# Kernel tuning notes

Measured on AMD Instinct MI355X. Metric: run time of the kernel, lower is better.

The kernel has to match this reference:

```python
import jax, jax.numpy as jnp
import numpy as np

D = 512       # d_model
L = 4         # num_layers
NH = 4        # nhead (fixed in __init__)
HD = D // NH
FF = 2 * D    # dim_feedforward = d_model*2
A = 32        # action_dim
B = 1024
STEPS = 64
SF_TH = 2.0   # sf_threshold
ALPHA = 2.0   # ATan surrogate width


@jax.custom_vjp
def spike(v):
    # Heaviside spike; surrogate gradient defined below (standard SNN practice)
    return (v > 0.0).astype(v.dtype)

def _spike_fwd(v):
    return spike(v), v

def _spike_bwd(v, g):
    sg = ALPHA / (2.0 * (1.0 + (jnp.pi / 2.0 * ALPHA * v) ** 2))
    return (g * sg,)

spike.defvjp(_spike_fwd, _spike_bwd)


def layer_norm(x, g, b):
    m = jnp.mean(x, axis=-1, keepdims=True)
    v = jnp.var(x, axis=-1, keepdims=True)
    return (x - m) / jnp.sqrt(v + 1e-5) * g + b


def setup_inputs() -> dict:
    key = jax.random.key(0)
    ks = jax.random.split(key, 24)
    w = lambda k, shape: jax.random.normal(k, shape, jnp.float32) * 0.02
    return {
        'initial_state': jax.random.normal(ks[0], (B, D), jnp.float32),
        'action_sequence': jax.random.normal(ks[1], (B, STEPS, A), jnp.float32),
        # action encoder
        'Wa': w(ks[2], (A, D)), 'ba': jnp.zeros((D,), jnp.float32),
        # per-layer SFormerBlock params, stacked on leading L dim
        'ln1_g': jnp.ones((L, D), jnp.float32), 'ln1_b': jnp.zeros((L, D), jnp.float32),
        'Wq': w(ks[3], (L, D, D)), 'bq': jnp.zeros((L, D), jnp.float32),
        'Wk': w(ks[4], (L, D, D)), 'bk': jnp.zeros((L, D), jnp.float32),
        'Wv': w(ks[5], (L, D, D)), 'bv': jnp.zeros((L, D), jnp.float32),
        'Wo': w(ks[6], (L, D, D)), 'bo': jnp.zeros((L, D), jnp.float32),
        'ln2_g': jnp.ones((L, D), jnp.float32), 'ln2_b': jnp.zeros((L, D), jnp.float32),
        'Wf1': w(ks[7], (L, D, FF)), 'bf1': jnp.zeros((L, FF), jnp.float32),
        'Wf2': w(ks[8], (L, FF, D)), 'bf2': jnp.zeros((L, D), jnp.float32),
        # transition AdaptiveLIFNeuron per-feature threshold
        'lif_th': jnp.ones((D,), jnp.float32),
        # reward head
        'Wr': w(ks[9], (D, 1)), 'br': jnp.zeros((1,), jnp.float32),
    }


def reference(initial_state, action_sequence, Wa, ba, ln1_g, ln1_b, Wq, bq, Wk, bk, Wv, bv, Wo, bo, ln2_g, ln2_b, Wf1, bf1, Wf2, bf2, lif_th, Wr, br):
    scale = 1.0 / jnp.sqrt(jnp.asarray(HD, jnp.float32))

    def block(x, l):
        # x: [B, 1, D]
        h = layer_norm(x, ln1_g[l], ln1_b[l])
        b_ = x.shape[0]
        q = (h @ Wq[l] + bq[l]).reshape(b_, 1, NH, HD)
        k = (h @ Wk[l] + bk[l]).reshape(b_, 1, NH, HD)
        v = (h @ Wv[l] + bv[l]).reshape(b_, 1, NH, HD)
        scores = jnp.einsum('bqhd,bkhd->bhqk', q, k) * scale
        attn = jax.nn.softmax(scores, axis=-1)
        o = jnp.einsum('bhqk,bkhd->bqhd', attn, v).reshape(b_, 1, D)
        x = x + o @ Wo[l] + bo[l]
        h2 = layer_norm(x, ln2_g[l], ln2_b[l])
        # spiking FFN: heaviside at sf_threshold with surrogate grad
        x = x + spike(h2 @ Wf1[l] + bf1[l] - SF_TH) @ Wf2[l] + bf2[l]
        return x

    def step(state, a):
        # predict_next_step
        x = state + a @ Wa + ba            # [B, D]
        x = x[:, None, :]                  # [B, 1, D]
        for l in range(L):
            x = block(x, l)
        x = x[:, 0, :]
        next_state = spike(x - lif_th)     # transition_lif (single-step LIF: v = input)
        reward = next_state @ Wr + br      # [B, 1]
        return next_state, (next_state, reward)

    acts = jnp.swapaxes(action_sequence, 0, 1)  # [Steps, B, A]
    final_state, (S, R) = jax.lax.scan(step, initial_state, acts)
    states = jnp.swapaxes(S, 0, 1)    # [B, Steps, D]
    rewards = jnp.swapaxes(R, 0, 1)   # [B, Steps, 1]
    return states, rewards, final_state
```

## Files before the change

### kernel.cpp

```cpp
#include <hip/hip_runtime.h>

#define D_ 512
#define FF_ 1024
#define L_ 4
#define A_ 32
#define B_ 1024
#define STEPS_ 64
#define RB_ 0.0625f
#define RB8_ 0.15f

typedef __attribute__((ext_vector_type(8))) short bf16x8;
typedef __attribute__((ext_vector_type(4))) float f32x4;
typedef __attribute__((ext_vector_type(2))) unsigned long u64x2;
#define MFMA16(a,b,c) __builtin_amdgcn_mfma_f32_16x16x32_bf16(a,b,c,0,0,0)
#define MFMA8(a,b,c)  __builtin_amdgcn_mfma_f32_16x16x32_fp8_fp8((long)(a),(long)(b),(c),0,0,0)

__device__ __forceinline__ unsigned rne16(float f) {
    unsigned u = __float_as_uint(f);
    return (u + 0x7fffu + ((u >> 16) & 1u)) >> 16;
}
__device__ __forceinline__ float fb(unsigned hu) { return __uint_as_float(hu << 16); }

#define LD4(R0, R1, R2, R3, P0_, P1_, P2_, P3_)                                \
    asm volatile("global_load_dwordx4 %0, %4, off\n\t"                         \
                 "global_load_dwordx4 %1, %5, off\n\t"                         \
                 "global_load_dwordx4 %2, %6, off\n\t"                         \
                 "global_load_dwordx4 %3, %7, off"                             \
                 : "=&v"(R0), "=&v"(R1), "=&v"(R2), "=&v"(R3)                  \
                 : "v"(P0_), "v"(P1_), "v"(P2_), "v"(P3_))

#define WAIT4(N, R0, R1, R2, R3)                                               \
    asm volatile("s_waitcnt vmcnt(" #N ")"                                     \
                 : "+v"(R0), "+v"(R1), "+v"(R2), "+v"(R3) :: "memory")

__global__ __launch_bounds__(256) void wvo_kernel(
    const float* __restrict__ Wv, const float* __restrict__ Wo,
    unsigned* __restrict__ Whi, unsigned* __restrict__ Wlo)
{
    __shared__ float wvt[16][D_];
    int bx  = blockIdx.x;
    int l   = bx >> 6;
    int rem = bx & 63;
    int k0  = (rem >> 1) * 16;
    int n   = (rem & 1) * 256 + threadIdx.x;

    const float* wvbase = Wv + (size_t)l * D_ * D_ + (size_t)k0 * D_;
    for (int idx = threadIdx.x; idx < 16 * D_; idx += 256)
        wvt[idx >> 9][idx & (D_ - 1)] = wvbase[idx];
    __syncthreads();

    float acc[16];
#pragma unroll
    for (int kk = 0; kk < 16; ++kk) acc[kk] = 0.f;

    const float* wop = Wo + (size_t)l * D_ * D_ + n;
    for (int m = 0; m < D_; m += 4) {
        float w0 = wop[(m + 0) * D_];
        float w1 = wop[(m + 1) * D_];
        float w2 = wop[(m + 2) * D_];
        float w3 = wop[(m + 3) * D_];
#pragma unroll
        for (int kk = 0; kk < 16; ++kk) {
            float4 wv4 = *(const float4*)&wvt[kk][m];
            acc[kk] += wv4.x * w0 + wv4.y * w1 + wv4.z * w2 + wv4.w * w3;
        }
    }
    int nt = n >> 4, ln15 = n & 15;
    int kkblk = k0 >> 5;
    int gbase = (k0 & 31) >> 3;
#pragma unroll
    for (int gi = 0; gi < 2; ++gi) {
        int lane_s = ((gbase + gi) << 4) | ln15;
        size_t fbase = ((((size_t)l * 32 + nt) * 16 + kkblk) * 64 + lane_s) * 4;
#pragma unroll
        for (int jp = 0; jp < 4; ++jp) {
            float v0 = acc[gi * 8 + jp * 2], v1 = acc[gi * 8 + jp * 2 + 1];
            unsigned h0 = rne16(v0), h1 = rne16(v1);
            Whi[fbase + jp] = h0 | (h1 << 16);
            float r0 = v0 - fb(h0), r1 = v1 - fb(h1);
            Wlo[fbase + jp] = rne16(r0) | (rne16(r1) << 16);
        }
    }
}

__global__ __launch_bounds__(256) void bvo_kernel(
    const float* __restrict__ bv, const float* __restrict__ bo,
    const float* __restrict__ Wo, float* __restrict__ bvo)
{
    int l = blockIdx.x >> 1;
    int n = (blockIdx.x & 1) * 256 + threadIdx.x;
    float acc = bo[l * D_ + n];
    const float* wop = Wo + (size_t)l * D_ * D_ + n;
    const float* bvp = bv + l * D_;
    for (int m = 0; m < D_; ++m) acc += bvp[m] * wop[m * D_];
    bvo[l * D_ + n] = acc;
}

__global__ __launch_bounds__(64) void packwf1_fp8(
    const float* __restrict__ Wf1, unsigned char* __restrict__ Pf8)
{
    int bid = blockIdx.x;
    int lane = threadIdx.x;
    int l  = bid >> 9;
    int nt = (bid >> 3) & 63;
    int p  = bid & 7;
    int n  = nt * 16 + (lane & 15);
    unsigned w[4];
#pragma unroll
    for (int half = 0; half < 2; ++half) {
        int kk = 2 * p + half;
        int krow = kk * 32 + (lane >> 4) * 8;
        const float* src = Wf1 + ((size_t)l * D_ + krow) * FF_ + n;
        float f0 = src[0 * FF_] * 16.f, f1 = src[1 * FF_] * 16.f;
        float f2 = src[2 * FF_] * 16.f, f3 = src[3 * FF_] * 16.f;
        float f4 = src[4 * FF_] * 16.f, f5 = src[5 * FF_] * 16.f;
        float f6 = src[6 * FF_] * 16.f, f7 = src[7 * FF_] * 16.f;
        unsigned lo = 0, hi = 0;
        lo = __builtin_amdgcn_cvt_pk_fp8_f32(f0, f1, lo, false);
        lo = __builtin_amdgcn_cvt_pk_fp8_f32(f2, f3, lo, true);
        hi = __builtin_amdgcn_cvt_pk_fp8_f32(f4, f5, hi, false);
        hi = __builtin_amdgcn_cvt_pk_fp8_f32(f6, f7, hi, true);
        w[half * 2] = lo; w[half * 2 + 1] = hi;
    }
    uint4 o; o.x = w[0]; o.y = w[1]; o.z = w[2]; o.w = w[3];
    ((uint4*)Pf8)[((size_t)(l * 64 + nt) * 8 + p) * 64 + lane] = o;
}

__device__ __forceinline__ void layer_norm_frag(
    float (*xb)[D_], unsigned* __restrict__ afrag,
    const float* __restrict__ g, const float* __restrict__ bt,
    float (*red)[4][2], int sg, int r)
{
    int c = 2 * r;
    float v0 = xb[sg][c], v1 = xb[sg][c + 1];
    float s  = v0 + v1;
    float ss = v0 * v0 + v1 * v1;
#pragma unroll
    for (int m = 1; m < 64; m <<= 1) {
        s  += __shfl_xor(s, m);
        ss += __shfl_xor(ss, m);
    }
    if ((r & 63) == 0) { red[sg][r >> 6][0] = s; red[sg][r >> 6][1] = ss; }
    __syncthreads();
    float S  = red[sg][0][0] + red[sg][1][0] + red[sg][2][0] + red[sg][3][0];
    float SS = red[sg][0][1] + red[sg][1][1] + red[sg][2][1] + red[sg][3][1];
    float mean = S * (1.f / 512.f);
    float var  = SS * (1.f / 512.f) - mean * mean;
    float rstd = 1.0f / sqrtf(var + 1e-5f);
    float h0 = (v0 - mean) * rstd * g[c]     + bt[c];
    float h1 = (v1 - mean) * rstd * g[c + 1] + bt[c + 1];
    unsigned u0 = rne16(h0), u1 = rne16(h1);
    float l0 = h0 - fb(u0), l1 = h1 - fb(u1);
    int kk = c >> 5, grp = (c & 31) >> 3, jp = (c & 7) >> 1;
    afrag[(kk * 64 + ((grp << 4) | sg))       * 4 + jp] = u0 | (u1 << 16);
    afrag[(kk * 64 + ((grp << 4) | (sg + 4))) * 4 + jp] = rne16(l0) | (rne16(l1) << 16);
    __syncthreads();
}

__device__ __forceinline__ void ln2_pack8(
    float (*xb)[D_], unsigned short* __restrict__ afrag8,
    const float* __restrict__ g, const float* __restrict__ bt,
    float (*red)[4][2], float* __restrict__ ln2m, float* __restrict__ ln2r,
    int sg, int r)
{
    int c = 2 * r;
    float v0 = xb[sg][c], v1 = xb[sg][c + 1];
    float s  = v0 + v1;
    float ss = v0 * v0 + v1 * v1;
#pragma unroll
    for (int m = 1; m < 64; m <<= 1) {
        s  += __shfl_xor(s, m);
        ss += __shfl_xor(ss, m);
    }
    if ((r & 63) == 0) { red[sg][r >> 6][0] = s; red[sg][r >> 6][1] = ss; }
    __syncthreads();
    float S  = red[sg][0][0] + red[sg][1][0] + red[sg][2][0] + red[sg][3][0];
    float SS = red[sg][0][1] + red[sg][1][1] + red[sg][2][1] + red[sg][3][1];
    float mean = S * (1.f / 512.f);
    float var  = SS * (1.f / 512.f) - mean * mean;
    float rstd = 1.0f / sqrtf(var + 1e-5f);
    if (r == 0) { ln2m[sg] = mean; ln2r[sg] = rstd; }
    float h0 = (v0 - mean) * rstd * g[c]     + bt[c];
    float h1 = (v1 - mean) * rstd * g[c + 1] + bt[c + 1];
    unsigned u = __builtin_amdgcn_cvt_pk_fp8_f32(h0, h1, 0, false);
    int kk = c >> 5, grp = (c & 31) >> 3, j = c & 7;
    afrag8[(kk * 64 + ((grp << 4) | sg)) * 4 + (j >> 1)] = (unsigned short)u;
    __syncthreads();
}

__global__ __launch_bounds__(1024)
__attribute__((amdgpu_waves_per_eu(4, 4)))
void smain(
    const float* __restrict__ init_state,
    const float* __restrict__ acts,
    const float* __restrict__ Wa,  const float* __restrict__ ba,
    const float* __restrict__ ln1g, const float* __restrict__ ln1b,
    const float* __restrict__ ln2g, const float* __restrict__ ln2b,
    const float* __restrict__ Wf1, const float* __restrict__ bf1,
    const float* __restrict__ Wf2, const float* __restrict__ bf2,
    const float* __restrict__ lifth,
    const float* __restrict__ Wr,  const float* __restrict__ br,
    const unsigned* __restrict__ Whi, const unsigned* __restrict__ Wlo,
    const unsigned char* __restrict__ Pf8, const float* __restrict__ bvo,
    float* __restrict__ out_states, float* __restrict__ out_rewards,
    float* __restrict__ out_final)
{
    __shared__ __align__(16) unsigned afrag[16 * 64 * 4];
    __shared__ __align__(16) unsigned short afrag8[16 * 64 * 4];
    __shared__ __align__(16) float xb[4][D_];
    __shared__ float areg[4][A_];
    __shared__ float red[4][4][2];
    __shared__ float rr[16];
    __shared__ float ln2m[4], ln2r[4];
    __shared__ int   fire_cnt, resc_cnt;
    __shared__ int   fire_list[256];
    __shared__ int   rescue_list[64];

    const int tid  = threadIdx.x;
    const int sg   = tid >> 8;
    const int r    = tid & 255;
    const int wv   = tid >> 6;
    const int lane = tid & 63;
    const int b    = blockIdx.x * 4 + sg;

    float st0 = init_state[(size_t)b * D_ + r];
    float st1 = init_state[(size_t)b * D_ + r + 256];
#pragma unroll
    for (int z = 0; z < 4; ++z) afrag[tid + z * 1024] = 0;
    ((unsigned*)afrag8)[tid] = 0;
    ((unsigned*)afrag8)[tid + 1024] = 0;
    __syncthreads();

    for (int t = 0; t < STEPS_; ++t) {
        if (tid < 128) {
            int sg2 = tid >> 5, j = tid & 31;
            areg[sg2][j] = acts[((size_t)(blockIdx.x * 4 + sg2)) * (STEPS_ * A_) + t * A_ + j];
        }
        __syncthreads();

        {
            float x0 = st0 + ba[r];
            float x1 = st1 + ba[r + 256];
#pragma unroll
            for (int j = 0; j < A_; ++j) {
                float av = areg[sg][j];
                x0 += av * Wa[j * D_ + r];
                x1 += av * Wa[j * D_ + r + 256];
            }
            xb[sg][r] = x0; xb[sg][r + 256] = x1;
        }
        __syncthreads();

        for (int l = 0; l < L_; ++l) {
            layer_norm_frag(xb, afrag, ln1g + l * D_, ln1b + l * D_, red, sg, r);

            {
                const bf16x8* Ah = (const bf16x8*)afrag;
                const size_t lb = (size_t)l * (32 * 16 * 64);
                const bf16x8* BH0 = (const bf16x8*)Whi + lb + (size_t)(2 * wv) * (16 * 64) + lane;
                const bf16x8* BL0 = (const bf16x8*)Wlo + lb + (size_t)(2 * wv) * (16 * 64) + lane;
                const bf16x8* BH1 = BH0 + 16 * 64;
                const bf16x8* BL1 = BL0 + 16 * 64;
                f32x4 c1a = {0.f,0.f,0.f,0.f}, c2a = c1a, c1b = c1a, c2b = c1a;
                bf16x8 aH0, aG0, aH1, aG1;
                bf16x8 bH0, bG0, bH1, bG1;
                bf16x8 cH0, cG0, cH1, cG1;
#define G1LD(S, KK) LD4(S##H0, S##G0, S##H1, S##G1, \
                        BH0 + (KK) * 64, BL0 + (KK) * 64, BH1 + (KK) * 64, BL1 + (KK) * 64)
#define G1MM(S, KK) do { bf16x8 a_ = Ah[(KK) * 64 + lane]; \
    c1a = MFMA16(a_, S##H0, c1a); c2a = MFMA16(a_, S##G0, c2a); \
    c1b = MFMA16(a_, S##H1, c1b); c2b = MFMA16(a_, S##G1, c2b); } while (0)
#define G1W(N, S) WAIT4(N, S##H0, S##G0, S##H1, S##G1)
                G1LD(a, 0); G1LD(b, 1); G1LD(c, 2);
                G1W(8, a); G1MM(a, 0);  G1LD(a, 3);
                G1W(8, b); G1MM(b, 1);  G1LD(b, 4);
                G1W(8, c); G1MM(c, 2);  G1LD(c, 5);
                G1W(8, a); G1MM(a, 3);  G1LD(a, 6);
                G1W(8, b); G1MM(b, 4);  G1LD(b, 7);
                G1W(8, c); G1MM(c, 5);  G1LD(c, 8);
                G1W(8, a); G1MM(a, 6);  G1LD(a, 9);
                G1W(8, b); G1MM(b, 7);  G1LD(b, 10);
                G1W(8, c); G1MM(c, 8);  G1LD(c, 11);
                G1W(8, a); G1MM(a, 9);  G1LD(a, 12);
                G1W(8, b); G1MM(b, 10); G1LD(b, 13);
                G1W(8, c); G1MM(c, 11); G1LD(c, 14);
                G1W(8, a); G1MM(a, 12); G1LD(a, 15);
                G1W(8, b); G1MM(b, 13);
                G1W(4, c); G1MM(c, 14);
                G1W(0, a); G1MM(a, 15);
#undef G1LD
#undef G1MM
#undef G1W
                const int nt0 = 2 * wv, nt1 = nt0 + 1;
#pragma unroll
                for (int s = 0; s < 4; ++s) {
                    float pa = c1a[s] + c2a[s]; float qa = __shfl(pa, (lane & 15) + 16);
                    float pb = c1b[s] + c2b[s]; float qb = __shfl(pb, (lane & 15) + 16);
                    if (lane < 16) {
                        int ca = nt0 * 16 + lane, cb = nt1 * 16 + lane;
                        xb[s][ca] += pa + qa + bvo[l * D_ + ca];
                        xb[s][cb] += pb + qb + bvo[l * D_ + cb];
                    }
                }
            }
            __syncthreads();

            if (tid == 0) { fire_cnt = 0; resc_cnt = 0; }

            ln2_pack8(xb, afrag8, ln2g + l * D_, ln2b + l * D_, red, ln2m, ln2r, sg, r);

            {
                const unsigned long* Ah8 = (const unsigned long*)afrag8;
                const int m0 = 4 * wv;
                const u64x2* Q0 = (const u64x2*)Pf8 + ((size_t)(l * 64 + m0 + 0) * 8) * 64 + lane;
                const u64x2* Q1 = (const u64x2*)Pf8 + ((size_t)(l * 64 + m0 + 1) * 8) * 64 + lane;
                const u64x2* Q2 = (const u64x2*)Pf8 + ((size_t)(l * 64 + m0 + 2) * 8) * 64 + lane;
                const u64x2* Q3 = (const u64x2*)Pf8 + ((size_t)(l * 64 + m0 + 3) * 8) * 64 + lane;
                f32x4 p0 = {0.f,0.f,0.f,0.f}, p1 = p0, p2 = p0, p3 = p0;
                u64x2 aB0, aB1, aB2, aB3;
                u64x2 bB0, bB1, bB2, bB3;
                u64x2 cB0, cB1, cB2, cB3;
#define G2LD(S, P) LD4(S##B0, S##B1, S##B2, S##B3, \
                       Q0 + (P) * 64, Q1 + (P) * 64, Q2 + (P) * 64, Q3 + (P) * 64)
#define G2MM(S, P) do { \
    unsigned long a0_ = Ah8[(2 * (P))     * 64 + lane]; \
    unsigned long a1_ = Ah8[(2 * (P) + 1) * 64 + lane]; \
    p0 = MFMA8(a0_, S##B0.x, p0); p1 = MFMA8(a0_, S##B1.x, p1); \
    p2 = MFMA8(a0_, S##B2.x, p2); p3 = MFMA8(a0_, S##B3.x, p3); \
    p0 = MFMA8(a1_, S##B0.y, p0); p1 = MFMA8(a1_, S##B1.y, p1); \
    p2 = MFMA8(a1_, S##B2.y, p2); p3 = MFMA8(a1_, S##B3.y, p3); } while (0)
#define G2W(N, S) WAIT4(N, S##B0, S##B1, S##B2, S##B3)
                G2LD(a, 0); G2LD(b, 1); G2LD(c, 2);
                G2W(8, a); G2MM(a, 0); G2LD(a, 3);
                G2W(8, b); G2MM(b, 1); G2LD(b, 4);
                G2W(8, c); G2MM(c, 2); G2LD(c, 5);
                G2W(8, a); G2MM(a, 3); G2LD(a, 6);
                G2W(8, b); G2MM(b, 4); G2LD(b, 7);
                G2W(8, c); G2MM(c, 5);
                G2W(4, a); G2MM(a, 6);
                G2W(0, b); G2MM(b, 7);
#undef G2LD
#undef G2MM
#undef G2W
                const float* bf1g = bf1 + l * FF_;
#pragma unroll
                for (int s = 0; s < 4; ++s) {
                    float v0 = p0[s]; float w0 = __shfl(v0, (lane & 15) + 16);
                    float v1 = p1[s]; float w1 = __shfl(v1, (lane & 15) + 16);
                    float v2 = p2[s]; float w2 = __shfl(v2, (lane & 15) + 16);
                    float v3 = p3[s]; float w3 = __shfl(v3, (lane & 15) + 16);
                    if (lane < 16) {
#pragma unroll
                        for (int q = 0; q < 4; ++q) {
                            float sum = (q == 0) ? v0 + w0 : (q == 1) ? v1 + w1
                                       : (q == 2) ? v2 + w2 : v3 + w3;
                            int n = (m0 + q) * 16 + lane;
                            float pr = sum * 0.0625f + bf1g[n] - 2.0f;
                            if (pr > RB8_) {
                                int idx = atomicAdd(&fire_cnt, 1);
                                if (idx < 256) fire_list[idx] = (s << 12) | n;
                            } else if (pr > -RB8_) {
                                int idx = atomicAdd(&resc_cnt, 1);
                                if (idx < 64) rescue_list[idx] = (s << 12) | n;
                            }
                        }
                    }
                }
            }
            __syncthreads();

            {
                int rc = resc_cnt; if (rc > 64) rc = 64;
                const float* g2 = ln2g + l * D_;
                const float* b2 = ln2b + l * D_;
                for (int e = 0; e < rc; ++e) {
                    int ent = rescue_list[e];
                    int i = ent >> 12, n = ent & 4095;
                    float p = 0.f;
                    if (tid < D_) {
                        float hh = (xb[i][tid] - ln2m[i]) * ln2r[i] * g2[tid] + b2[tid];
                        p = hh * Wf1[((size_t)l * D_ + tid) * FF_ + n];
                    }
#pragma unroll
                    for (int m = 1; m < 64; m <<= 1) p += __shfl_xor(p, m);
                    if ((tid & 63) == 0) rr[tid >> 6] = p;
                    __syncthreads();
                    if (tid == 0) {
                        float dot = 0.f;
#pragma unroll
                        for (int w = 0; w < 8; ++w) dot += rr[w];
                        float pre = dot + bf1[l * FF_ + n] - 2.0f;
                        if (pre > 0.f) {
                            int idx = atomicAdd(&fire_cnt, 1);
                            if (idx < 256) fire_list[idx] = ent;
                        }
                    }
                    __syncthreads();
                }
            }

            {
                int cnt = fire_cnt; if (cnt > 256) cnt = 256;
                if (cnt > 0) {
                    for (int e = 0; e < cnt; ++e) {
                        int ent = fire_list[e];
                        int i = ent >> 12, n = ent & 4095;
                        if (tid < D_) xb[i][tid] += Wf2[(size_t)l * (FF_ * D_) + (size_t)n * D_ + tid];
                    }
                    __syncthreads();
                }
                xb[sg][r]       += bf2[l * D_ + r];
                xb[sg][r + 256] += bf2[l * D_ + r + 256];
            }
            __syncthreads();
        }

        {
            float x0 = xb[sg][r], x1 = xb[sg][r + 256];
            float s0 = (x0 > lifth[r])       ? 1.0f : 0.0f;
            float s1 = (x1 > lifth[r + 256]) ? 1.0f : 0.0f;
            st0 = s0; st1 = s1;
            size_t so = ((size_t)b * STEPS_ + t) * D_;
            __builtin_nontemporal_store(s0, &out_states[so + r]);
            __builtin_nontemporal_store(s1, &out_states[so + r + 256]);

            float rs = s0 * Wr[r] + s1 * Wr[r + 256];
#pragma unroll
            for (int m = 1; m < 64; m <<= 1) rs += __shfl_xor(rs, m);
            if ((r & 63) == 0) red[sg][r >> 6][0] = rs;
            __syncthreads();
            if (r == 0)
                __builtin_nontemporal_store(
                    red[sg][0][0] + red[sg][1][0] + red[sg][2][0] + red[sg][3][0] + br[0],
                    &out_rewards[(size_t)b * STEPS_ + t]);
        }
        __syncthreads();
    }

    __builtin_nontemporal_store(st0, &out_final[(size_t)b * D_ + r]);
    __builtin_nontemporal_store(st1, &out_final[(size_t)b * D_ + r + 256]);
}

extern "C" void kernel_launch(void* const* d_in, const int* in_sizes, int n_in,
                              void* d_out, int out_size, void* d_ws, size_t ws_size,
                              hipStream_t stream) {
    (void)in_sizes; (void)n_in; (void)out_size; (void)ws_size;
    const float* init_state = (const float*)d_in[0];
    const float* acts  = (const float*)d_in[1];
    const float* Wa    = (const float*)d_in[2];
    const float* ba    = (const float*)d_in[3];
    const float* ln1g  = (const float*)d_in[4];
    const float* ln1b  = (const float*)d_in[5];
    const float* Wv    = (const float*)d_in[10];
    const float* bv    = (const float*)d_in[11];
    const float* Wo    = (const float*)d_in[12];
    const float* bo    = (const float*)d_in[13];
    const float* ln2g  = (const float*)d_in[14];
    const float* ln2b  = (const float*)d_in[15];
    const float* Wf1   = (const float*)d_in[16];
    const float* bf1   = (const float*)d_in[17];
    const float* Wf2   = (const float*)d_in[18];
    const float* bf2   = (const float*)d_in[19];
    const float* lifth = (const float*)d_in[20];
    const float* Wr    = (const float*)d_in[21];
    const float* br    = (const float*)d_in[22];

    unsigned* Whi = (unsigned*)d_ws;
    unsigned* Wlo = Whi + 524288;
    unsigned char* Pf8 = (unsigned char*)(Wlo + 524288);
    float*    bvo = (float*)(Pf8 + 2097152);

    float* out         = (float*)d_out;
    float* out_states  = out;
    float* out_rewards = out + (size_t)B_ * STEPS_ * D_;
    float* out_final   = out_rewards + (size_t)B_ * STEPS_;

    wvo_kernel<<<dim3(256), dim3(256), 0, stream>>>(Wv, Wo, Whi, Wlo);
    bvo_kernel<<<dim3(8),   dim3(256), 0, stream>>>(bv, bo, Wo, bvo);
    packwf1_fp8<<<dim3(2048), dim3(64), 0, stream>>>(Wf1, Pf8);
    smain<<<dim3(256), dim3(1024), 0, stream>>>(
        init_state, acts, Wa, ba, ln1g, ln1b, ln2g, ln2b,
        Wf1, bf1, Wf2, bf2, lifth, Wr, br, Whi, Wlo, Pf8, bvo,
        out_states, out_rewards, out_final);
}
```

Measured before the change: 7.067 ms.

## Prefetch GEMM weights across layernorm, use LDS-only barriers, cache params in LDS

Result: slower. 7.429 ms (+5.1%).

```diff
diff --git a/kernel.cpp b/kernel.cpp
--- a/kernel.cpp
+++ b/kernel.cpp
@@ -6,7 +6,6 @@
 #define A_ 32
 #define B_ 1024
 #define STEPS_ 64
-#define RB_ 0.0625f
 #define RB8_ 0.15f
 
 typedef __attribute__((ext_vector_type(8))) short bf16x8;
@@ -20,6 +19,12 @@
     return (u + 0x7fffu + ((u >> 16) & 1u)) >> 16;
 }
 __device__ __forceinline__ float fb(unsigned hu) { return __uint_as_float(hu << 16); }
+
+__device__ __forceinline__ void syncl() {
+    asm volatile("s_waitcnt lgkmcnt(0)" ::: "memory");
+    __builtin_amdgcn_s_barrier();
+    asm volatile("" ::: "memory");
+}
 
 #define LD4(R0, R1, R2, R3, P0_, P1_, P2_, P3_)                                \
     asm volatile("global_load_dwordx4 %0, %4, off\n\t"                         \
@@ -141,7 +146,7 @@
         ss += __shfl_xor(ss, m);
     }
     if ((r & 63) == 0) { red[sg][r >> 6][0] = s; red[sg][r >> 6][1] = ss; }
-    __syncthreads();
+    syncl();
     float S  = red[sg][0][0] + red[sg][1][0] + red[sg][2][0] + red[sg][3][0];
     float SS = red[sg][0][1] + red[sg][1][1] + red[sg][2][1] + red[sg][3][1];
     float mean = S * (1.f / 512.f);
@@ -154,7 +159,7 @@
     int kk = c >> 5, grp = (c & 31) >> 3, jp = (c & 7) >> 1;
     afrag[(kk * 64 + ((grp << 4) | sg))       * 4 + jp] = u0 | (u1 << 16);
     afrag[(kk * 64 + ((grp << 4) | (sg + 4))) * 4 + jp] = rne16(l0) | (rne16(l1) << 16);
-    __syncthreads();
+    syncl();
 }
 
 __device__ __forceinline__ void ln2_pack8(
@@ -173,7 +178,7 @@
         ss += __shfl_xor(ss, m);
     }
     if ((r & 63) == 0) { red[sg][r >> 6][0] = s; red[sg][r >> 6][1] = ss; }
-    __syncthreads();
+    syncl();
     float S  = red[sg][0][0] + red[sg][1][0] + red[sg][2][0] + red[sg][3][0];
     float SS = red[sg][0][1] + red[sg][1][1] + red[sg][2][1] + red[sg][3][1];
     float mean = S * (1.f / 512.f);
@@ -185,7 +190,7 @@
     unsigned u = __builtin_amdgcn_cvt_pk_fp8_f32(h0, h1, 0, false);
     int kk = c >> 5, grp = (c & 31) >> 3, j = c & 7;
     afrag8[(kk * 64 + ((grp << 4) | sg)) * 4 + (j >> 1)] = (unsigned short)u;
-    __syncthreads();
+    syncl();
 }
 
 __global__ __launch_bounds__(1024)
@@ -208,6 +213,11 @@
     __shared__ __align__(16) unsigned afrag[16 * 64 * 4];
     __shared__ __align__(16) unsigned short afrag8[16 * 64 * 4];
     __shared__ __align__(16) float xb[4][D_];
+    __shared__ __align__(16) float pg1[L_][D_], pb1[L_][D_];
+    __shared__ __align__(16) float pg2[L_][D_], pb2[L_][D_];
+    __shared__ __align__(16) float pbvo[L_][D_], pbf2[L_][D_];
+    __shared__ __align__(16) float pbf1m2[L_][FF_];
+    __shared__ __align__(16) float plif[D_], pba[D_], pwr[D_];
     __shared__ float areg[4][A_];
     __shared__ float red[4][4][2];
     __shared__ float rr[16];
@@ -225,6 +235,13 @@
 
     float st0 = init_state[(size_t)b * D_ + r];
     float st1 = init_state[(size_t)b * D_ + r + 256];
+    for (int i = tid; i < L_ * D_; i += 1024) {
+        ((float*)pg1)[i]  = ln1g[i];  ((float*)pb1)[i]  = ln1b[i];
+        ((float*)pg2)[i]  = ln2g[i];  ((float*)pb2)[i]  = ln2b[i];
+        ((float*)pbvo)[i] = bvo[i];   ((float*)pbf2)[i] = bf2[i];
+    }
+    for (int i = tid; i < L_ * FF_; i += 1024) ((float*)pbf1m2)[i] = bf1[i] - 2.0f;
+    if (tid < D_) { plif[tid] = lifth[tid]; pba[tid] = ba[tid]; pwr[tid] = Wr[tid]; }
 #pragma unroll
     for (int z = 0; z < 4; ++z) afrag[tid + z * 1024] = 0;
     ((unsigned*)afrag8)[tid] = 0;
@@ -236,11 +253,11 @@
             int sg2 = tid >> 5, j = tid & 31;
             areg[sg2][j] = acts[((size_t)(blockIdx.x * 4 + sg2)) * (STEPS_ * A_) + t * A_ + j];
         }
-        __syncthreads();
+        syncl();
 
         {
-            float x0 = st0 + ba[r];
-            float x1 = st1 + ba[r + 256];
+            float x0 = st0 + pba[r];
+            float x1 = st1 + pba[r + 256];
 #pragma unroll
             for (int j = 0; j < A_; ++j) {
                 float av = areg[sg][j];
@@ -249,29 +266,30 @@
             }
             xb[sg][r] = x0; xb[sg][r + 256] = x1;
         }
-        __syncthreads();
+        syncl();
 
         for (int l = 0; l < L_; ++l) {
-            layer_norm_frag(xb, afrag, ln1g + l * D_, ln1b + l * D_, red, sg, r);
-
-            {
-                const bf16x8* Ah = (const bf16x8*)afrag;
-                const size_t lb = (size_t)l * (32 * 16 * 64);
-                const bf16x8* BH0 = (const bf16x8*)Whi + lb + (size_t)(2 * wv) * (16 * 64) + lane;
-                const bf16x8* BL0 = (const bf16x8*)Wlo + lb + (size_t)(2 * wv) * (16 * 64) + lane;
-                const bf16x8* BH1 = BH0 + 16 * 64;
-                const bf16x8* BL1 = BL0 + 16 * 64;
-                f32x4 c1a = {0.f,0.f,0.f,0.f}, c2a = c1a, c1b = c1a, c2b = c1a;
-                bf16x8 aH0, aG0, aH1, aG1;
-                bf16x8 bH0, bG0, bH1, bG1;
-                bf16x8 cH0, cG0, cH1, cG1;
+            const bf16x8* Ah = (const bf16x8*)afrag;
+            const size_t lb = (size_t)l * (32 * 16 * 64);
+            const bf16x8* BH0 = (const bf16x8*)Whi + lb + (size_t)(2 * wv) * (16 * 64) + lane;
+            const bf16x8* BL0 = (const bf16x8*)Wlo + lb + (size_t)(2 * wv) * (16 * 64) + lane;
+            const bf16x8* BH1 = BH0 + 16 * 64;
+            const bf16x8* BL1 = BL0 + 16 * 64;
+            bf16x8 aH0, aG0, aH1, aG1;
+            bf16x8 bH0, bG0, bH1, bG1;
+            bf16x8 cH0, cG0, cH1, cG1;
 #define G1LD(S, KK) LD4(S##H0, S##G0, S##H1, S##G1, \
                         BH0 + (KK) * 64, BL0 + (KK) * 64, BH1 + (KK) * 64, BL1 + (KK) * 64)
 #define G1MM(S, KK) do { bf16x8 a_ = Ah[(KK) * 64 + lane]; \
     c1a = MFMA16(a_, S##H0, c1a); c2a = MFMA16(a_, S##G0, c2a); \
     c1b = MFMA16(a_, S##H1, c1b); c2b = MFMA16(a_, S##G1, c2b); } while (0)
 #define G1W(N, S) WAIT4(N, S##H0, S##G0, S##H1, S##G1)
-                G1LD(a, 0); G1LD(b, 1); G1LD(c, 2);
+            G1LD(a, 0); G1LD(b, 1); G1LD(c, 2);
+
+            layer_norm_frag(xb, afrag, &pg1[l][0], &pb1[l][0], red, sg, r);
+
+            {
+                f32x4 c1a = {0.f,0.f,0.f,0.f}, c2a = c1a, c1b = c1a, c2b = c1a;
                 G1W(8, a); G1MM(a, 0);  G1LD(a, 3);
                 G1W(8, b); G1MM(b, 1);  G1LD(b, 4);
                 G1W(8, c); G1MM(c, 2);  G1LD(c, 5);
@@ -288,9 +306,6 @@
                 G1W(8, b); G1MM(b, 13);
                 G1W(4, c); G1MM(c, 14);
                 G1W(0, a); G1MM(a, 15);
-#undef G1LD
-#undef G1MM
-#undef G1W
                 const int nt0 = 2 * wv, nt1 = nt0 + 1;
 #pragma unroll
                 for (int s = 0; s < 4; ++s) {
@@ -298,28 +313,27 @@
                     float pb = c1b[s] + c2b[s]; float qb = __shfl(pb, (lane & 15) + 16);
                     if (lane < 16) {
                         int ca = nt0 * 16 + lane, cb = nt1 * 16 + lane;
-                        xb[s][ca] += pa + qa + bvo[l * D_ + ca];
-                        xb[s][cb] += pb + qb + bvo[l * D_ + cb];
+                        xb[s][ca] += pa + qa + pbvo[l][ca];
+                        xb[s][cb] += pb + qb + pbvo[l][cb];
                     }
                 }
             }
-            __syncthreads();
+#undef G1LD
+#undef G1MM
+#undef G1W
+            syncl();
 
             if (tid == 0) { fire_cnt = 0; resc_cnt = 0; }
 
-            ln2_pack8(xb, afrag8, ln2g + l * D_, ln2b + l * D_, red, ln2m, ln2r, sg, r);
-
-            {
-                const unsigned long* Ah8 = (const unsigned long*)afrag8;
-                const int m0 = 4 * wv;
-                const u64x2* Q0 = (const u64x2*)Pf8 + ((size_t)(l * 64 + m0 + 0) * 8) * 64 + lane;
-                const u64x2* Q1 = (const u64x2*)Pf8 + ((size_t)(l * 64 + m0 + 1) * 8) * 64 + lane;
-                const u64x2* Q2 = (const u64x2*)Pf8 + ((size_t)(l * 64 + m0 + 2) * 8) * 64 + lane;
-                const u64x2* Q3 = (const u64x2*)Pf8 + ((size_t)(l * 64 + m0 + 3) * 8) * 64 + lane;
-                f32x4 p0 = {0.f,0.f,0.f,0.f}, p1 = p0, p2 = p0, p3 = p0;
-                u64x2 aB0, aB1, aB2, aB3;
-                u64x2 bB0, bB1, bB2, bB3;
-                u64x2 cB0, cB1, cB2, cB3;
+            const unsigned long* Ah8 = (const unsigned long*)afrag8;
+            const int m0 = 4 * wv;
+            const u64x2* Q0 = (const u64x2*)Pf8 + ((size_t)(l * 64 + m0 + 0) * 8) * 64 + lane;
+            const u64x2* Q1 = (const u64x2*)Pf8 + ((size_t)(l * 64 + m0 + 1) * 8) * 64 + lane;
+            const u64x2* Q2 = (const u64x2*)Pf8 + ((size_t)(l * 64 + m0 + 2) * 8) * 64 + lane;
+            const u64x2* Q3 = (const u64x2*)Pf8 + ((size_t)(l * 64 + m0 + 3) * 8) * 64 + lane;
+            u64x2 aB0, aB1, aB2, aB3;
+            u64x2 bB0, bB1, bB2, bB3;
+            u64x2 cB0, cB1, cB2, cB3;
 #define G2LD(S, P) LD4(S##B0, S##B1, S##B2, S##B3, \
                        Q0 + (P) * 64, Q1 + (P) * 64, Q2 + (P) * 64, Q3 + (P) * 64)
 #define G2MM(S, P) do { \
@@ -330,7 +344,12 @@
     p0 = MFMA8(a1_, S##B0.y, p0); p1 = MFMA8(a1_, S##B1.y, p1); \
     p2 = MFMA8(a1_, S##B2.y, p2); p3 = MFMA8(a1_, S##B3.y, p3); } while (0)
 #define G2W(N, S) WAIT4(N, S##B0, S##B1, S##B2, S##B3)
-                G2LD(a, 0); G2LD(b, 1); G2LD(c, 2);
+            G2LD(a, 0); G2LD(b, 1); G2LD(c, 2);
+
+            ln2_pack8(xb, afrag8, &pg2[l][0], &pb2[l][0], red, ln2m, ln2r, sg, r);
+
+            {
+                f32x4 p0 = {0.f,0.f,0.f,0.f}, p1 = p0, p2 = p0, p3 = p0;
                 G2W(8, a); G2MM(a, 0); G2LD(a, 3);
                 G2W(8, b); G2MM(b, 1); G2LD(b, 4);
                 G2W(8, c); G2MM(c, 2); G2LD(c, 5);
@@ -339,10 +358,6 @@
                 G2W(8, c); G2MM(c, 5);
                 G2W(4, a); G2MM(a, 6);
                 G2W(0, b); G2MM(b, 7);
-#undef G2LD
-#undef G2MM
-#undef G2W
-                const float* bf1g = bf1 + l * FF_;
 #pragma unroll
                 for (int s = 0; s < 4; ++s) {
                     float v0 = p0[s]; float w0 = __shfl(v0, (lane & 15) + 16);
@@ -355,7 +370,7 @@
                             float sum = (q == 0) ? v0 + w0 : (q == 1) ? v1 + w1
                                        : (q == 2) ? v2 + w2 : v3 + w3;
                             int n = (m0 + q) * 16 + lane;
-                            float pr = sum * 0.0625f + bf1g[n] - 2.0f;
+                            float pr = sum * 0.0625f + pbf1m2[l][n];
                             if (pr > RB8_) {
                                 int idx = atomicAdd(&fire_cnt, 1);
                                 if (idx < 256) fire_list[idx] = (s << 12) | n;
@@ -367,12 +382,15 @@
                     }
                 }
             }
-            __syncthreads();
+#undef G2LD
+#undef G2MM
+#undef G2W
+            syncl();
 
             {
                 int rc = resc_cnt; if (rc > 64) rc = 64;
-                const float* g2 = ln2g + l * D_;
-                const float* b2 = ln2b + l * D_;
+                const float* g2 = &pg2[l][0];
+                const float* b2 = &pb2[l][0];
                 for (int e = 0; e < rc; ++e) {
                     int ent = rescue_list[e];
                     int i = ent >> 12, n = ent & 4095;
@@ -384,7 +402,7 @@
 #pragma unroll
                     for (int m = 1; m < 64; m <<= 1) p += __shfl_xor(p, m);
                     if ((tid & 63) == 0) rr[tid >> 6] = p;
-                    __syncthreads();
+                    syncl();
                     if (tid == 0) {
                         float dot = 0.f;
 #pragma unroll
@@ -395,7 +413,7 @@
                             if (idx < 256) fire_list[idx] = ent;
                         }
                     }
-                    __syncthreads();
+                    syncl();
                 }
             }
 
@@ -407,34 +425,34 @@
                         int i = ent >> 12, n = ent & 4095;
                         if (tid < D_) xb[i][tid] += Wf2[(size_t)l * (FF_ * D_) + (size_t)n * D_ + tid];
                     }
-                    __syncthreads();
+                    syncl();
                 }
-                xb[sg][r]       += bf2[l * D_ + r];
-                xb[sg][r + 256] += bf2[l * D_ + r + 256];
+                xb[sg][r]       += pbf2[l][r];
+                xb[sg][r + 256] += pbf2[l][r + 256];
             }
-            __syncthreads();
+            syncl();
         }
 
         {
             float x0 = xb[sg][r], x1 = xb[sg][r + 256];
-            float s0 = (x0 > lifth[r])       ? 1.0f : 0.0f;
-            float s1 = (x1 > lifth[r + 256]) ? 1.0f : 0.0f;
+            float s0 = (x0 > plif[r])       ? 1.0f : 0.0f;
+            float s1 = (x1 > plif[r + 256]) ? 1.0f : 0.0f;
             st0 = s0; st1 = s1;
             size_t so = ((size_t)b * STEPS_ + t) * D_;
             __builtin_nontemporal_store(s0, &out_states[so + r]);
             __builtin_nontemporal_store(s1, &out_states[so + r + 256]);
 
-            float rs = s0 * Wr[r] + s1 * Wr[r + 256];
+            float rs = s0 * pwr[r] + s1 * pwr[r + 256];
 #pragma unroll
             for (int m = 1; m < 64; m <<= 1) rs += __shfl_xor(rs, m);
             if ((r & 63) == 0) red[sg][r >> 6][0] = rs;
-            __syncthreads();
+            syncl();
             if (r == 0)
                 __builtin_nontemporal_store(
                     red[sg][0][0] + red[sg][1][0] + red[sg][2][0] + red[sg][3][0] + br[0],
                     &out_rewards[(size_t)b * STEPS_ + t]);
         }
-        __syncthreads();
+        syncl();
     }
 
     __builtin_nontemporal_store(st0, &out_final[(size_t)b * D_ + r]);
```

## Split persistent kernel into 512 blocks of 2 batch rows each

Applied to the files above, without the earlier changes.

Result: slower. 9.574 ms (+35.5%).

```diff
diff --git a/kernel.cpp b/kernel.cpp
--- a/kernel.cpp
+++ b/kernel.cpp
@@ -6,7 +6,6 @@
 #define A_ 32
 #define B_ 1024
 #define STEPS_ 64
-#define RB_ 0.0625f
 #define RB8_ 0.15f
 
 typedef __attribute__((ext_vector_type(8))) short bf16x8;
@@ -188,9 +187,7 @@
     __syncthreads();
 }
 
-__global__ __launch_bounds__(1024)
-__attribute__((amdgpu_waves_per_eu(4, 4)))
-void smain(
+__global__ __launch_bounds__(512, 4) void smain(
     const float* __restrict__ init_state,
     const float* __restrict__ acts,
     const float* __restrict__ Wa,  const float* __restrict__ ba,
@@ -207,11 +204,11 @@
 {
     __shared__ __align__(16) unsigned afrag[16 * 64 * 4];
     __shared__ __align__(16) unsigned short afrag8[16 * 64 * 4];
-    __shared__ __align__(16) float xb[4][D_];
-    __shared__ float areg[4][A_];
-    __shared__ float red[4][4][2];
-    __shared__ float rr[16];
-    __shared__ float ln2m[4], ln2r[4];
+    __shared__ __align__(16) float xb[2][D_];
+    __shared__ float areg[2][A_];
+    __shared__ float red[2][4][2];
+    __shared__ float rr[8];
+    __shared__ float ln2m[2], ln2r[2];
     __shared__ int   fire_cnt, resc_cnt;
     __shared__ int   fire_list[256];
     __shared__ int   rescue_list[64];
@@ -221,20 +218,20 @@
     const int r    = tid & 255;
     const int wv   = tid >> 6;
     const int lane = tid & 63;
-    const int b    = blockIdx.x * 4 + sg;
+    const int b    = blockIdx.x * 2 + sg;
 
     float st0 = init_state[(size_t)b * D_ + r];
     float st1 = init_state[(size_t)b * D_ + r + 256];
 #pragma unroll
-    for (int z = 0; z < 4; ++z) afrag[tid + z * 1024] = 0;
-    ((unsigned*)afrag8)[tid] = 0;
-    ((unsigned*)afrag8)[tid + 1024] = 0;
+    for (int z = 0; z < 8; ++z) afrag[tid + z * 512] = 0;
+#pragma unroll
+    for (int z = 0; z < 4; ++z) ((unsigned*)afrag8)[tid + z * 512] = 0;
     __syncthreads();
 
     for (int t = 0; t < STEPS_; ++t) {
-        if (tid < 128) {
+        if (tid < 64) {
             int sg2 = tid >> 5, j = tid & 31;
-            areg[sg2][j] = acts[((size_t)(blockIdx.x * 4 + sg2)) * (STEPS_ * A_) + t * A_ + j];
+            areg[sg2][j] = acts[((size_t)(blockIdx.x * 2 + sg2)) * (STEPS_ * A_) + t * A_ + j];
         }
         __syncthreads();
 
@@ -254,11 +251,12 @@
         for (int l = 0; l < L_; ++l) {
             layer_norm_frag(xb, afrag, ln1g + l * D_, ln1b + l * D_, red, sg, r);
 
-            {
+            for (int pass = 0; pass < 2; ++pass) {
                 const bf16x8* Ah = (const bf16x8*)afrag;
                 const size_t lb = (size_t)l * (32 * 16 * 64);
-                const bf16x8* BH0 = (const bf16x8*)Whi + lb + (size_t)(2 * wv) * (16 * 64) + lane;
-                const bf16x8* BL0 = (const bf16x8*)Wlo + lb + (size_t)(2 * wv) * (16 * 64) + lane;
+                const int ntb = 4 * wv + 2 * pass;
+                const bf16x8* BH0 = (const bf16x8*)Whi + lb + (size_t)ntb * (16 * 64) + lane;
+                const bf16x8* BL0 = (const bf16x8*)Wlo + lb + (size_t)ntb * (16 * 64) + lane;
                 const bf16x8* BH1 = BH0 + 16 * 64;
                 const bf16x8* BL1 = BL0 + 16 * 64;
                 f32x4 c1a = {0.f,0.f,0.f,0.f}, c2a = c1a, c1b = c1a, c2b = c1a;
@@ -291,13 +289,12 @@
 #undef G1LD
 #undef G1MM
 #undef G1W
-                const int nt0 = 2 * wv, nt1 = nt0 + 1;
-#pragma unroll
-                for (int s = 0; s < 4; ++s) {
+#pragma unroll
+                for (int s = 0; s < 2; ++s) {
                     float pa = c1a[s] + c2a[s]; float qa = __shfl(pa, (lane & 15) + 16);
                     float pb = c1b[s] + c2b[s]; float qb = __shfl(pb, (lane & 15) + 16);
                     if (lane < 16) {
-                        int ca = nt0 * 16 + lane, cb = nt1 * 16 + lane;
+                        int ca = ntb * 16 + lane, cb = (ntb + 1) * 16 + lane;
                         xb[s][ca] += pa + qa + bvo[l * D_ + ca];
                         xb[s][cb] += pb + qb + bvo[l * D_ + cb];
                     }
@@ -309,9 +306,9 @@
 
             ln2_pack8(xb, afrag8, ln2g + l * D_, ln2b + l * D_, red, ln2m, ln2r, sg, r);
 
-            {
+            for (int pass = 0; pass < 2; ++pass) {
                 const unsigned long* Ah8 = (const unsigned long*)afrag8;
-                const int m0 = 4 * wv;
+                const int m0 = 8 * wv + 4 * pass;
                 const u64x2* Q0 = (const u64x2*)Pf8 + ((size_t)(l * 64 + m0 + 0) * 8) * 64 + lane;
                 const u64x2* Q1 = (const u64x2*)Pf8 + ((size_t)(l * 64 + m0 + 1) * 8) * 64 + lane;
                 const u64x2* Q2 = (const u64x2*)Pf8 + ((size_t)(l * 64 + m0 + 2) * 8) * 64 + lane;
@@ -344,7 +341,7 @@
 #undef G2W
                 const float* bf1g = bf1 + l * FF_;
 #pragma unroll
-                for (int s = 0; s < 4; ++s) {
+                for (int s = 0; s < 2; ++s) {
                     float v0 = p0[s]; float w0 = __shfl(v0, (lane & 15) + 16);
                     float v1 = p1[s]; float w1 = __shfl(v1, (lane & 15) + 16);
                     float v2 = p2[s]; float w2 = __shfl(v2, (lane & 15) + 16);
@@ -376,11 +373,8 @@
                 for (int e = 0; e < rc; ++e) {
                     int ent = rescue_list[e];
                     int i = ent >> 12, n = ent & 4095;
-                    float p = 0.f;
-                    if (tid < D_) {
-                        float hh = (xb[i][tid] - ln2m[i]) * ln2r[i] * g2[tid] + b2[tid];
-                        p = hh * Wf1[((size_t)l * D_ + tid) * FF_ + n];
-                    }
+                    float hh = (xb[i][tid] - ln2m[i]) * ln2r[i] * g2[tid] + b2[tid];
+                    float p = hh * Wf1[((size_t)l * D_ + tid) * FF_ + n];
 #pragma unroll
                     for (int m = 1; m < 64; m <<= 1) p += __shfl_xor(p, m);
                     if ((tid & 63) == 0) rr[tid >> 6] = p;
@@ -405,7 +399,7 @@
                     for (int e = 0; e < cnt; ++e) {
                         int ent = fire_list[e];
                         int i = ent >> 12, n = ent & 4095;
-                        if (tid < D_) xb[i][tid] += Wf2[(size_t)l * (FF_ * D_) + (size_t)n * D_ + tid];
+                        xb[i][tid] += Wf2[(size_t)l * (FF_ * D_) + (size_t)n * D_ + tid];
                     }
                     __syncthreads();
                 }
@@ -478,7 +472,7 @@
     wvo_kernel<<<dim3(256), dim3(256), 0, stream>>>(Wv, Wo, Whi, Wlo);
     bvo_kernel<<<dim3(8),   dim3(256), 0, stream>>>(bv, bo, Wo, bvo);
     packwf1_fp8<<<dim3(2048), dim3(64), 0, stream>>>(Wf1, Pf8);
-    smain<<<dim3(256), dim3(1024), 0, stream>>>(
+    smain<<<dim3(512), dim3(512), 0, stream>>>(
         init_state, acts, Wa, ba, ln1g, ln1b, ln2g, ln2b,
         Wf1, bf1, Wf2, bf2, lifth, Wr, br, Whi, Wlo, Pf8, bvo,
         out_states, out_rewards, out_final);
```
